# Kernel tuning notes

Measured on AMD Instinct MI355X. Metric: run time of the kernel, lower is better.

## Reference

```python
import jax, jax.numpy as jnp
import numpy as np

H = 100      # hidden/embedding size (hard-coded in the module)
HD = H // 2  # per-direction encoder hidden
V = 50000


def lstm_scan(xs, h0, c0, Wx, Wh, b):
    """xs: [T,B,E] -> (all hidden states [T,B,H], final h, final c)."""
    def step(carry, x):
        h, c = carry
        g = x @ Wx + h @ Wh + b          # [B, 4H]
        i, f, gg, o = jnp.split(g, 4, axis=-1)
        c = jax.nn.sigmoid(f) * c + jax.nn.sigmoid(i) * jnp.tanh(gg)
        h = jax.nn.sigmoid(o) * jnp.tanh(c)
        return (h, c), h
    (h, c), hs = jax.lax.scan(step, (h0, c0), xs)
    return hs, h, c


def setup_inputs() -> dict:
    key = jax.random.key(0)
    ks = jax.random.split(key, 16)
    B, S, T = 128, 512, 128
    s = 0.02
    inp = {
        "src": jax.random.randint(ks[0], (B, S), 0, V),
        "tgt": jax.random.randint(ks[1], (B, T), 0, V),
        "mask_src": jnp.ones((B, S), dtype=bool),
        "emb": jax.random.normal(ks[2], (V, H), jnp.float32) * s,
        "demb": jax.random.normal(ks[3], (V, H), jnp.float32) * s,
        "enc_Wx_f": jax.random.normal(ks[4], (H, 4 * HD), jnp.float32) * s,
        "enc_Wh_f": jax.random.normal(ks[5], (HD, 4 * HD), jnp.float32) * s,
        "enc_b_f": jnp.zeros((4 * HD,), jnp.float32),
        "enc_Wx_b": jax.random.normal(ks[6], (H, 4 * HD), jnp.float32) * s,
        "enc_Wh_b": jax.random.normal(ks[7], (HD, 4 * HD), jnp.float32) * s,
        "enc_b_b": jnp.zeros((4 * HD,), jnp.float32),
        "dec_Wx": jax.random.normal(ks[8], (H, 4 * H), jnp.float32) * s,
        "dec_Wh": jax.random.normal(ks[9], (H, 4 * H), jnp.float32) * s,
        "dec_b": jnp.zeros((4 * H,), jnp.float32),
        "Wa": jax.random.normal(ks[10], (H, H), jnp.float32) * s,
        "Wc": jax.random.normal(ks[11], (2 * H, H), jnp.float32) * s,
    }
    return inp


def reference(src, tgt, mask_src, emb, demb,
              enc_Wx_f, enc_Wh_f, enc_b_f,
              enc_Wx_b, enc_Wh_b, enc_b_b,
              dec_Wx, dec_Wh, dec_b, Wa, Wc):
    B, S = src.shape
    # ---- bidirectional LSTM encoder ----
    x = emb[src].transpose(1, 0, 2)                      # [S,B,H]
    z = jnp.zeros((B, HD), x.dtype)
    hf, hfT, cfT = lstm_scan(x, z, z, enc_Wx_f, enc_Wh_f, enc_b_f)
    hb_r, hbT, cbT = lstm_scan(x[::-1], z, z, enc_Wx_b, enc_Wh_b, enc_b_b)
    hb = hb_r[::-1]
    mem = jnp.concatenate([hf, hb], -1).transpose(1, 0, 2)  # [B,S,H] memory bank
    h0 = jnp.concatenate([hfT, hbT], -1)                 # [B,H] init decoder state
    c0 = jnp.concatenate([cfT, cbT], -1)
    # ---- LSTM decoder (teacher forcing on tgt[:, :-1]) ----
    y = demb[tgt[:, :-1]].transpose(1, 0, 2)             # [T-1,B,H]
    dh, _, _ = lstm_scan(y, h0, c0, dec_Wx, dec_Wh, dec_b)
    dh = dh.transpose(1, 0, 2)                           # [B,T-1,H]
    # ---- global (general/Luong) attention over memory bank ----
    scores = jnp.einsum('bth,hk,bsk->bts', dh, Wa, mem)  # [B,T-1,S]
    scores = jnp.where(mask_src[:, None, :], scores, -1e9)
    attn = jax.nn.softmax(scores, axis=-1)
    ctx = jnp.einsum('bts,bsh->bth', attn, mem)          # [B,T-1,H]
    decode_output = jnp.tanh(jnp.concatenate([dh, ctx], -1) @ Wc)  # [B,T-1,H]
    return decode_output, attn
```

## Files before the change

kernel.cpp:

```cpp
#include <hip/hip_runtime.h>
#include <hip/hip_bf16.h>

#define B_   128
#define S_   512
#define TM1  127
#define H_   100
#define HD_  50

__device__ __forceinline__ float sigm(float x) {
    return __fdividef(1.0f, 1.0f + __expf(-x));
}
__device__ __forceinline__ float ftanh(float x) {
    float e = __expf(2.0f * x);
    return __fdividef(e - 1.0f, e + 1.0f);
}
__device__ __forceinline__ void wave_barrier() {
    __builtin_amdgcn_sched_barrier(0);
    asm volatile("s_waitcnt lgkmcnt(0)");
    __builtin_amdgcn_sched_barrier(0);
    __builtin_amdgcn_s_barrier();
    __builtin_amdgcn_sched_barrier(0);
}

__global__ __launch_bounds__(256) void k_xg_enc(
    const int* __restrict__ src, const float* __restrict__ emb,
    const float* __restrict__ Wf, const float* __restrict__ bf,
    const float* __restrict__ Wb, const float* __restrict__ bb,
    float* __restrict__ xgfT, float* __restrict__ xgbT)
{
    __shared__ __align__(16) float a[32][100];
    __shared__ int ridx[32];
    const int tid = threadIdx.x;
    const int b   = blockIdx.x & 127;
    const int t0  = (blockIdx.x >> 7) * 32;
    if (tid < 32) ridx[tid] = src[b * S_ + t0 + tid];
    __syncthreads();
    for (int i = tid; i < 32 * 100; i += 256) {
        int rr = i / 100, k = i - rr * 100;
        a[rr][k] = emb[(size_t)ridx[rr] * 100 + k];
    }
    __syncthreads();
    #pragma unroll
    for (int pass = 0; pass < 2; ++pass) {
        int j = tid + pass * 256;
        if (j < 400) {
            const float* W; const float* bias; float* out; int jj;
            if (j < 200) { W = Wf; bias = bf; out = xgfT; jj = j; }
            else         { W = Wb; bias = bb; out = xgbT; jj = j - 200; }
            float acc[32];
            float bv = bias[jj];
            #pragma unroll
            for (int rr = 0; rr < 32; ++rr) acc[rr] = bv;
            for (int k4 = 0; k4 < 25; ++k4) {
                float w0 = W[(4 * k4 + 0) * 200 + jj];
                float w1 = W[(4 * k4 + 1) * 200 + jj];
                float w2 = W[(4 * k4 + 2) * 200 + jj];
                float w3 = W[(4 * k4 + 3) * 200 + jj];
                #pragma unroll
                for (int rr = 0; rr < 32; ++rr) {
                    float4 av = reinterpret_cast<const float4*>(a[rr])[k4];
                    acc[rr] = fmaf(av.x, w0, acc[rr]);
                    acc[rr] = fmaf(av.y, w1, acc[rr]);
                    acc[rr] = fmaf(av.z, w2, acc[rr]);
                    acc[rr] = fmaf(av.w, w3, acc[rr]);
                }
            }
            const int gate = jj / 50, uu = jj - (jj / 50) * 50;
            const int pj = uu * 4 + gate;
            float* dst = out + ((size_t)b * 200 + pj) * 512 + t0;
            #pragma unroll
            for (int q = 0; q < 8; ++q)
                *reinterpret_cast<float4*>(dst + 4 * q) =
                    make_float4(acc[4*q+0], acc[4*q+1], acc[4*q+2], acc[4*q+3]);
        }
    }
}

__global__ __launch_bounds__(256) void k_xg_dec(
    const int* __restrict__ tgt, const float* __restrict__ demb,
    const float* __restrict__ W, const float* __restrict__ bias,
    float* __restrict__ xgdT)
{
    __shared__ __align__(16) float a[32][100];
    __shared__ int ridx[32];
    const int tid = threadIdx.x;
    const int b   = blockIdx.x & 127;
    const int t0  = (blockIdx.x >> 7) * 32;
    if (tid < 32) ridx[tid] = tgt[b * 128 + t0 + tid];
    __syncthreads();
    for (int i = tid; i < 32 * 100; i += 256) {
        int rr = i / 100, k = i - rr * 100;
        a[rr][k] = demb[(size_t)ridx[rr] * 100 + k];
    }
    __syncthreads();
    #pragma unroll
    for (int pass = 0; pass < 2; ++pass) {
        int j = tid + pass * 256;
        if (j < 400) {
            float acc[32];
            float bv = bias[j];
            #pragma unroll
            for (int rr = 0; rr < 32; ++rr) acc[rr] = bv;
            for (int k4 = 0; k4 < 25; ++k4) {
                float w0 = W[(4 * k4 + 0) * 400 + j];
                float w1 = W[(4 * k4 + 1) * 400 + j];
                float w2 = W[(4 * k4 + 2) * 400 + j];
                float w3 = W[(4 * k4 + 3) * 400 + j];
                #pragma unroll
                for (int rr = 0; rr < 32; ++rr) {
                    float4 av = reinterpret_cast<const float4*>(a[rr])[k4];
                    acc[rr] = fmaf(av.x, w0, acc[rr]);
                    acc[rr] = fmaf(av.y, w1, acc[rr]);
                    acc[rr] = fmaf(av.z, w2, acc[rr]);
                    acc[rr] = fmaf(av.w, w3, acc[rr]);
                }
            }
            const int gate = j / 100, uu = j - (j / 100) * 100;
            const int pj = uu * 4 + gate;
            float* dst = xgdT + ((size_t)b * 400 + pj) * 128 + t0;
            #pragma unroll
            for (int q = 0; q < 8; ++q)
                *reinterpret_cast<float4*>(dst + 4 * q) =
                    make_float4(acc[4*q+0], acc[4*q+1], acc[4*q+2], acc[4*q+3]);
        }
    }
}

__global__ __launch_bounds__(256, 1) void k_enc(
    const float* __restrict__ xgfT, const float* __restrict__ xgbT,
    const float* __restrict__ Whf, const float* __restrict__ Whb,
    float* __restrict__ memT, float* __restrict__ h0, float* __restrict__ c0)
{
    const int blk = blockIdx.x;
    const int dir = blk >> 7;
    const int b   = blk & 127;
    const float* __restrict__ xgT = dir ? xgbT : xgfT;
    const float* __restrict__ Wh  = dir ? Whb  : Whf;
    const int tid = threadIdx.x;
    const int u    = tid >> 2;
    const int gbit = tid & 3;
    const bool active = tid < 200;
    const bool glane  = active && (gbit == 0);

    __shared__ __align__(16) float hbuf[2][56];
    __shared__ float hT[2][50][17];

    const int col = active ? (gbit * 50 + u) : 0;
    const float* wbase = Wh + col;
    float4 W0,W1,W2,W3,W4,W5,W6,W7,W8,W9,W10,W11,W12;
#define LDW(i) \
    asm volatile("global_load_dword %0, %1, off" : "=v"(W##i.x) : "v"(wbase + (4*(i)+0)*200)); \
    asm volatile("global_load_dword %0, %1, off" : "=v"(W##i.y) : "v"(wbase + (4*(i)+1)*200)); \
    asm volatile("global_load_dword %0, %1, off" : "=v"(W##i.z) : "v"(wbase + (4*(i)+2)*200)); \
    asm volatile("global_load_dword %0, %1, off" : "=v"(W##i.w) : "v"(wbase + (4*(i)+3)*200));
    LDW(0) LDW(1) LDW(2) LDW(3) LDW(4) LDW(5) LDW(6)
    LDW(7) LDW(8) LDW(9) LDW(10) LDW(11)
#undef LDW
    asm volatile("global_load_dword %0, %1, off" : "=v"(W12.x) : "v"(wbase + 48*200));
    asm volatile("global_load_dword %0, %1, off" : "=v"(W12.y) : "v"(wbase + 49*200));
    asm volatile("s_waitcnt vmcnt(0)");
    __builtin_amdgcn_sched_barrier(0);
    W12.z = 0.f; W12.w = 0.f;

    if (tid < 56) { hbuf[0][tid] = 0.f; hbuf[1][tid] = 0.f; }
    float c = 0.f;
    wave_barrier();

    const float* xrow = xgT + ((size_t)b * 200 + (active ? tid : 0)) * 512;

#define LOADQ(g_) ((active && (g_) < 128) \
    ? *reinterpret_cast<const float4*>(xrow + (dir ? (508 - 4 * (g_)) : (4 * (g_)))) \
    : make_float4(0.f, 0.f, 0.f, 0.f))

#define EDOT(i, h4) { float4 hv = (h4)[i]; \
    a0 = fmaf(hv.x, W##i.x, a0); a1 = fmaf(hv.y, W##i.y, a1); \
    a2 = fmaf(hv.z, W##i.z, a2); a3 = fmaf(hv.w, W##i.w, a3); }

#define ESTEP(s_, rb_, gx_) { \
    float gv; \
    { \
        const float4* h4 = reinterpret_cast<const float4*>(hbuf[rb_]); \
        float a0 = 0.f, a1 = 0.f, a2 = 0.f, a3 = 0.f; \
        EDOT(0, h4) EDOT(1, h4) EDOT(2, h4) EDOT(3, h4) EDOT(4, h4) \
        EDOT(5, h4) EDOT(6, h4) EDOT(7, h4) EDOT(8, h4) EDOT(9, h4) \
        EDOT(10, h4) EDOT(11, h4) EDOT(12, h4) \
        gv = (gx_) + (a0 + a1) + (a2 + a3); \
    } \
    const float x1 = __shfl_xor(gv, 1); \
    const float x2 = __shfl_xor(gv, 2); \
    const float x3 = __shfl_xor(gv, 3); \
    const int t_ = dir ? (S_ - 1 - (s_)) : (s_); \
    if (glane) { \
        c = sigm(x1) * c + sigm(gv) * ftanh(x2); \
        float h = sigm(x3) * ftanh(c); \
        hbuf[(rb_) ^ 1][u] = h; \
        hT[((s_) >> 4) & 1][u][t_ & 15] = h; \
    } \
    wave_barrier(); \
    if (((s_) & 15) == 15) { \
        const int tbase = dir ? t_ : ((s_) - 15); \
        const int par = ((s_) >> 4) & 1; \
        for (int i = tid; i < 50 * 16; i += 256) { \
            int uu = i >> 4, tt = i & 15; \
            memT[((size_t)b * 100 + dir * 50 + uu) * 512 + tbase + tt] = \
                hT[par][uu][tt]; \
        } \
    } \
}

    float4 cq = LOADQ(0);
    for (int g = 0; g < 128; ++g) {
        const int s = g * 4;
        float4 nq = LOADQ(g + 1);
        if (dir) {
            ESTEP(s + 0, 0, cq.w)
            ESTEP(s + 1, 1, cq.z)
            ESTEP(s + 2, 0, cq.y)
            ESTEP(s + 3, 1, cq.x)
        } else {
            ESTEP(s + 0, 0, cq.x)
            ESTEP(s + 1, 1, cq.y)
            ESTEP(s + 2, 0, cq.z)
            ESTEP(s + 3, 1, cq.w)
        }
        cq = nq;
    }
#undef ESTEP
#undef EDOT
#undef LOADQ
    if (glane) {
        h0[b * 100 + dir * 50 + u] = hbuf[0][u];
        c0[b * 100 + dir * 50 + u] = c;
    }
}

__global__ __launch_bounds__(832, 1) void k_dec(
    const float* __restrict__ xgdT, const float* __restrict__ Whd,
    const float* __restrict__ h0v, const float* __restrict__ c0v,
    float* __restrict__ dh)
{
    const int b   = blockIdx.x;
    const int tid = threadIdx.x;
    const int u   = tid >> 3;
    const int gt  = (tid >> 1) & 3;
    const int p   = tid & 1;
    const bool active = tid < 800;
    const bool glane  = active && ((tid & 7) == 0);

    __shared__ __align__(16) float hbuf[2][100];

    const int colD = active ? (gt * 100 + u) : 0;
    const int pofs = active ? (p * 50) : 0;
    float2 V0,V1,V2,V3,V4,V5,V6,V7,V8,V9,V10,V11,V12,
           V13,V14,V15,V16,V17,V18,V19,V20,V21,V22,V23,V24;
#define LDV(i) V##i = make_float2(Whd[(size_t)(pofs + 2*i    ) * 400 + colD], \
                                  Whd[(size_t)(pofs + 2*i + 1) * 400 + colD]);
    LDV(0) LDV(1) LDV(2) LDV(3) LDV(4) LDV(5) LDV(6) LDV(7) LDV(8) LDV(9)
    LDV(10) LDV(11) LDV(12) LDV(13) LDV(14) LDV(15) LDV(16) LDV(17) LDV(18)
    LDV(19) LDV(20) LDV(21) LDV(22) LDV(23) LDV(24)
#undef LDV

    if (tid < 100) hbuf[0][tid] = h0v[b * 100 + tid];
    float c = 0.f;
    if (glane) c = c0v[b * 100 + u];
    wave_barrier();

    const float* xrow = xgdT + ((size_t)b * 400 + (tid >> 1)) * 128;

#define LOADQD(g_) ((active && p == 0 && (g_) < 32) \
    ? *reinterpret_cast<const float4*>(xrow + 4 * (g_)) \
    : make_float4(0.f, 0.f, 0.f, 0.f))

#define DDOT(i, h2) { float2 hv = (h2)[i]; \
    a0 = fmaf(hv.x, V##i.x, a0); a1 = fmaf(hv.y, V##i.y, a1); }

#define DSTEP(s_, rb_, gx_) { \
    float pv; \
    { \
        const float2* h2 = reinterpret_cast<const float2*>(hbuf[rb_] + p * 50); \
        float a0 = 0.f, a1 = 0.f; \
        DDOT(0, h2) DDOT(1, h2) DDOT(2, h2) DDOT(3, h2) DDOT(4, h2) \
        DDOT(5, h2) DDOT(6, h2) DDOT(7, h2) DDOT(8, h2) DDOT(9, h2) \
        DDOT(10, h2) DDOT(11, h2) DDOT(12, h2) DDOT(13, h2) DDOT(14, h2) \
        DDOT(15, h2) DDOT(16, h2) DDOT(17, h2) DDOT(18, h2) DDOT(19, h2) \
        DDOT(20, h2) DDOT(21, h2) DDOT(22, h2) DDOT(23, h2) DDOT(24, h2) \
        pv = a0 + a1; \
    } \
    pv += __shfl_xor(pv, 1); \
    const float gv = (gx_) + pv; \
    const float x2 = __shfl_xor(gv, 2); \
    const float x4 = __shfl_xor(gv, 4); \
    const float x6 = __shfl_xor(gv, 6); \
    if (glane) { \
        c = sigm(x2) * c + sigm(gv) * ftanh(x4); \
        float h = sigm(x6) * ftanh(c); \
        hbuf[(rb_) ^ 1][u] = h; \
        dh[((size_t)(s_) * 128 + b) * 100 + u] = h; \
    } \
    wave_barrier(); \
}

    float4 q0 = LOADQD(0);
    float4 q1 = LOADQD(1);
    int s = 0;
    for (int g = 0; g < 31; ++g) {
        float4 qc = q0; q0 = q1; q1 = LOADQD(g + 2);
        DSTEP(s + 0, 0, qc.x)
        DSTEP(s + 1, 1, qc.y)
        DSTEP(s + 2, 0, qc.z)
        DSTEP(s + 3, 1, qc.w)
        s += 4;
    }
    DSTEP(s + 0, 0, q0.x)
    DSTEP(s + 1, 1, q0.y)
    DSTEP(s + 2, 0, q0.z)
#undef DSTEP
#undef DDOT
#undef LOADQD
}

__global__ __launch_bounds__(128) void k_dhwa(
    const float* __restrict__ dh, const float* __restrict__ Wa,
    float* __restrict__ out)
{
    __shared__ __align__(16) float a[32][100];
    const int tid = threadIdx.x;
    const size_t r0 = (size_t)blockIdx.x * 32;
    for (int i = tid; i < 32 * 100; i += 128) {
        int rr = i / 100, k = i - rr * 100;
        a[rr][k] = dh[(r0 + rr) * 100 + k];
    }
    __syncthreads();
    if (tid < 100) {
        float acc[32];
        #pragma unroll
        for (int rr = 0; rr < 32; ++rr) acc[rr] = 0.f;
        for (int k4 = 0; k4 < 25; ++k4) {
            float w0 = Wa[(4 * k4 + 0) * 100 + tid];
            float w1 = Wa[(4 * k4 + 1) * 100 + tid];
            float w2 = Wa[(4 * k4 + 2) * 100 + tid];
            float w3 = Wa[(4 * k4 + 3) * 100 + tid];
            #pragma unroll
            for (int rr = 0; rr < 32; ++rr) {
                float4 av = reinterpret_cast<const float4*>(a[rr])[k4];
                acc[rr] = fmaf(av.x, w0, acc[rr]);
                acc[rr] = fmaf(av.y, w1, acc[rr]);
                acc[rr] = fmaf(av.z, w2, acc[rr]);
                acc[rr] = fmaf(av.w, w3, acc[rr]);
            }
        }
        #pragma unroll
        for (int rr = 0; rr < 32; ++rr) out[(r0 + rr) * 100 + tid] = acc[rr];
    }
}

__global__ __launch_bounds__(256) void k_attn(
    const float* __restrict__ dhWa, const float* __restrict__ memT,
    float* __restrict__ attn_out, float* __restrict__ ctx)
{
    const int tid = threadIdx.x;
    const int b   = blockIdx.x & 127;
    const int t0  = (blockIdx.x >> 7) * 8;
    const int nt  = (TM1 - t0 < 8) ? (TM1 - t0) : 8;
    __shared__ __align__(16) float q[8][100];
    __shared__ __align__(16) float p[8][512];
    __shared__ float redm[4][8];
    __shared__ float reds[4][8];
    for (int i = tid; i < 8 * 100; i += 256) {
        int rr = i / 100, k = i - rr * 100;
        q[rr][k] = (rr < nt) ? dhWa[((size_t)(t0 + rr) * 128 + b) * 100 + k] : 0.0f;
    }
    __syncthreads();
    float acc0[8], acc1[8];
    #pragma unroll
    for (int rr = 0; rr < 8; ++rr) { acc0[rr] = 0.f; acc1[rr] = 0.f; }
    const float* mb = memT + (size_t)b * 100 * 512;
    for (int k4 = 0; k4 < 25; ++k4) {
        float qs[8][4];
        #pragma unroll
        for (int rr = 0; rr < 8; ++rr) {
            float4 v = reinterpret_cast<const float4*>(q[rr])[k4];
            qs[rr][0] = v.x; qs[rr][1] = v.y; qs[rr][2] = v.z; qs[rr][3] = v.w;
        }
        #pragma unroll
        for (int uu = 0; uu < 4; ++uu) {
            const float* col = mb + (size_t)(4 * k4 + uu) * 512;
            float m0 = col[tid], m1 = col[tid + 256];
            #pragma unroll
            for (int rr = 0; rr < 8; ++rr) {
                acc0[rr] = fmaf(qs[rr][uu], m0, acc0[rr]);
                acc1[rr] = fmaf(qs[rr][uu], m1, acc1[rr]);
            }
        }
    }
    const int wid = tid >> 6;
    #pragma unroll
    for (int rr = 0; rr < 8; ++rr) {
        float m = fmaxf(acc0[rr], acc1[rr]);
        #pragma unroll
        for (int k = 1; k < 64; k <<= 1) m = fmaxf(m, __shfl_xor(m, k));
        if ((tid & 63) == 0) redm[wid][rr] = m;
    }
    __syncthreads();
    #pragma unroll
    for (int rr = 0; rr < 8; ++rr) {
        float m = fmaxf(fmaxf(redm[0][rr], redm[1][rr]),
                        fmaxf(redm[2][rr], redm[3][rr]));
        acc0[rr] = __expf(acc0[rr] - m);
        acc1[rr] = __expf(acc1[rr] - m);
        float s = acc0[rr] + acc1[rr];
        #pragma unroll
        for (int k = 1; k < 64; k <<= 1) s += __shfl_xor(s, k);
        if ((tid & 63) == 0) reds[wid][rr] = s;
    }
    __syncthreads();
    #pragma unroll
    for (int rr = 0; rr < 8; ++rr) {
        float s = (reds[0][rr] + reds[1][rr]) + (reds[2][rr] + reds[3][rr]);
        float inv = __fdividef(1.0f, s);
        float e0 = acc0[rr] * inv, e1 = acc1[rr] * inv;
        p[rr][tid] = e0; p[rr][tid + 256] = e1;
        if (rr < nt) {
            float* ao = attn_out + ((size_t)b * TM1 + t0 + rr) * 512;
            ao[tid] = e0; ao[tid + 256] = e1;
        }
    }
    __syncthreads();
    if (tid < 200) {
        const int h  = (tid < 100) ? tid : tid - 100;
        const int r0 = (tid < 100) ? 0 : 4;
        const float4* mrow = reinterpret_cast<const float4*>(mb + (size_t)h * 512);
        const float4* p0 = reinterpret_cast<const float4*>(p[r0 + 0]);
        const float4* p1 = reinterpret_cast<const float4*>(p[r0 + 1]);
        const float4* p2 = reinterpret_cast<const float4*>(p[r0 + 2]);
        const float4* p3 = reinterpret_cast<const float4*>(p[r0 + 3]);
        float a0 = 0.f, a1 = 0.f, a2 = 0.f, a3 = 0.f;
        for (int s4 = 0; s4 < 128; ++s4) {
            float4 mv = mrow[s4];
            float4 v0 = p0[s4], v1 = p1[s4], v2 = p2[s4], v3 = p3[s4];
            a0 = fmaf(v0.x, mv.x, a0); a0 = fmaf(v0.y, mv.y, a0);
            a0 = fmaf(v0.z, mv.z, a0); a0 = fmaf(v0.w, mv.w, a0);
            a1 = fmaf(v1.x, mv.x, a1); a1 = fmaf(v1.y, mv.y, a1);
            a1 = fmaf(v1.z, mv.z, a1); a1 = fmaf(v1.w, mv.w, a1);
            a2 = fmaf(v2.x, mv.x, a2); a2 = fmaf(v2.y, mv.y, a2);
            a2 = fmaf(v2.z, mv.z, a2); a2 = fmaf(v2.w, mv.w, a2);
            a3 = fmaf(v3.x, mv.x, a3); a3 = fmaf(v3.y, mv.y, a3);
            a3 = fmaf(v3.z, mv.z, a3); a3 = fmaf(v3.w, mv.w, a3);
        }
        float av[4] = {a0, a1, a2, a3};
        #pragma unroll
        for (int k = 0; k < 4; ++k) {
            int rr = r0 + k;
            if (rr < nt)
                ctx[((size_t)b * TM1 + t0 + rr) * 100 + h] = av[k];
        }
    }
}

__global__ __launch_bounds__(128) void k_final(
    const float* __restrict__ dh, const float* __restrict__ ctx,
    const float* __restrict__ Wc, float* __restrict__ outp)
{
    __shared__ __align__(16) float a[32][200];
    const int tid = threadIdx.x;
    const int r0 = blockIdx.x * 32;
    for (int i = tid; i < 32 * 200; i += 128) {
        int rr = i / 200, k = i - rr * 200;
        int r = r0 + rr; int bb = r / 127; int t = r - bb * 127;
        a[rr][k] = (k < 100) ? dh[((size_t)t * 128 + bb) * 100 + k]
                             : ctx[(size_t)r * 100 + (k - 100)];
    }
    __syncthreads();
    if (tid < 100) {
        float acc[32];
        #pragma unroll
        for (int rr = 0; rr < 32; ++rr) acc[rr] = 0.f;
        for (int k4 = 0; k4 < 50; ++k4) {
            float w0 = Wc[(4 * k4 + 0) * 100 + tid];
            float w1 = Wc[(4 * k4 + 1) * 100 + tid];
            float w2 = Wc[(4 * k4 + 2) * 100 + tid];
            float w3 = Wc[(4 * k4 + 3) * 100 + tid];
            #pragma unroll
            for (int rr = 0; rr < 32; ++rr) {
                float4 av = reinterpret_cast<const float4*>(a[rr])[k4];
                acc[rr] = fmaf(av.x, w0, acc[rr]);
                acc[rr] = fmaf(av.y, w1, acc[rr]);
                acc[rr] = fmaf(av.z, w2, acc[rr]);
                acc[rr] = fmaf(av.w, w3, acc[rr]);
            }
        }
        #pragma unroll
        for (int rr = 0; rr < 32; ++rr)
            outp[(size_t)(r0 + rr) * 100 + tid] = tanhf(acc[rr]);
    }
}

extern "C" void kernel_launch(void* const* d_in, const int* in_sizes, int n_in,
                              void* d_out, int out_size, void* d_ws, size_t ws_size,
                              hipStream_t stream) {
    const int*   src  = (const int*)d_in[0];
    const int*   tgt  = (const int*)d_in[1];
    const float* emb  = (const float*)d_in[3];
    const float* demb = (const float*)d_in[4];
    const float* Wxf  = (const float*)d_in[5];
    const float* Whf  = (const float*)d_in[6];
    const float* bf   = (const float*)d_in[7];
    const float* Wxb  = (const float*)d_in[8];
    const float* Whb  = (const float*)d_in[9];
    const float* bb   = (const float*)d_in[10];
    const float* Wxd  = (const float*)d_in[11];
    const float* Whd  = (const float*)d_in[12];
    const float* bd   = (const float*)d_in[13];
    const float* Wa   = (const float*)d_in[14];
    const float* Wc   = (const float*)d_in[15];

    float* ws    = (float*)d_ws;
    float* xgfT  = ws;
    float* xgbT  = xgfT + 13107200;
    float* xgdT  = xgbT + 13107200;
    float* memT  = xgdT + 6553600;
    float* h0    = memT + 6553600;
    float* c0    = h0 + 12800;
    float* dh    = ws;
    float* dhwa  = dh + 1625600;
    float* ctx   = dhwa + 1625600;

    float* out_dec  = (float*)d_out;
    float* out_attn = out_dec + 1625600;

    k_xg_enc<<<2048, 256, 0, stream>>>(src, emb, Wxf, bf, Wxb, bb, xgfT, xgbT);
    k_xg_dec<<<512, 256, 0, stream>>>(tgt, demb, Wxd, bd, xgdT);
    k_enc<<<256, 256, 0, stream>>>(xgfT, xgbT, Whf, Whb, memT, h0, c0);
    k_dec<<<128, 832, 0, stream>>>(xgdT, Whd, h0, c0, dh);
    k_dhwa<<<508, 128, 0, stream>>>(dh, Wa, dhwa);
    k_attn<<<2048, 256, 0, stream>>>(dhwa, memT, out_attn, ctx);
    k_final<<<508, 128, 0, stream>>>(dh, ctx, Wc, out_dec);
}
```

Baseline: 854.9 us.

## Fuse dh@Wa projection into attention kernel and merge projection passes per thread

The separate k_dhwa kernel is removed. Each attention block now computes its own 8-row dh·Wa query tile in shared memory before scoring, which drops one launch and the round trip of the intermediate through global memory. The input-gate projection kernels also change from two passes over 256 threads to one pass over 200 threads, each computing two output columns, so every shared-memory activation load feeds twice as many FMAs. The cost is higher register pressure (64 accumulators per thread), 56 idle threads per block, and a small amount of extra serial work at the start of each attention block.

Result: faster. 809.0 us (-5.4%).

```diff
diff --git a/kernel.cpp b/kernel.cpp
--- a/kernel.cpp
+++ b/kernel.cpp
@@ -40,38 +40,44 @@
         a[rr][k] = emb[(size_t)ridx[rr] * 100 + k];
     }
     __syncthreads();
-    #pragma unroll
-    for (int pass = 0; pass < 2; ++pass) {
-        int j = tid + pass * 256;
-        if (j < 400) {
-            const float* W; const float* bias; float* out; int jj;
-            if (j < 200) { W = Wf; bias = bf; out = xgfT; jj = j; }
-            else         { W = Wb; bias = bb; out = xgbT; jj = j - 200; }
-            float acc[32];
-            float bv = bias[jj];
-            #pragma unroll
-            for (int rr = 0; rr < 32; ++rr) acc[rr] = bv;
-            for (int k4 = 0; k4 < 25; ++k4) {
-                float w0 = W[(4 * k4 + 0) * 200 + jj];
-                float w1 = W[(4 * k4 + 1) * 200 + jj];
-                float w2 = W[(4 * k4 + 2) * 200 + jj];
-                float w3 = W[(4 * k4 + 3) * 200 + jj];
-                #pragma unroll
-                for (int rr = 0; rr < 32; ++rr) {
-                    float4 av = reinterpret_cast<const float4*>(a[rr])[k4];
-                    acc[rr] = fmaf(av.x, w0, acc[rr]);
-                    acc[rr] = fmaf(av.y, w1, acc[rr]);
-                    acc[rr] = fmaf(av.z, w2, acc[rr]);
-                    acc[rr] = fmaf(av.w, w3, acc[rr]);
-                }
+    if (tid < 200) {
+        const int jj = tid;
+        float accF[32], accB[32];
+        const float bvF = bf[jj], bvB = bb[jj];
+        #pragma unroll
+        for (int rr = 0; rr < 32; ++rr) { accF[rr] = bvF; accB[rr] = bvB; }
+        for (int k4 = 0; k4 < 25; ++k4) {
+            float f0 = Wf[(4 * k4 + 0) * 200 + jj];
+            float f1 = Wf[(4 * k4 + 1) * 200 + jj];
+            float f2 = Wf[(4 * k4 + 2) * 200 + jj];
+            float f3 = Wf[(4 * k4 + 3) * 200 + jj];
+            float g0 = Wb[(4 * k4 + 0) * 200 + jj];
+            float g1 = Wb[(4 * k4 + 1) * 200 + jj];
+            float g2 = Wb[(4 * k4 + 2) * 200 + jj];
+            float g3 = Wb[(4 * k4 + 3) * 200 + jj];
+            #pragma unroll
+            for (int rr = 0; rr < 32; ++rr) {
+                float4 av = reinterpret_cast<const float4*>(a[rr])[k4];
+                accF[rr] = fmaf(av.x, f0, accF[rr]);
+                accF[rr] = fmaf(av.y, f1, accF[rr]);
+                accF[rr] = fmaf(av.z, f2, accF[rr]);
+                accF[rr] = fmaf(av.w, f3, accF[rr]);
+                accB[rr] = fmaf(av.x, g0, accB[rr]);
+                accB[rr] = fmaf(av.y, g1, accB[rr]);
+                accB[rr] = fmaf(av.z, g2, accB[rr]);
+                accB[rr] = fmaf(av.w, g3, accB[rr]);
             }
-            const int gate = jj / 50, uu = jj - (jj / 50) * 50;
-            const int pj = uu * 4 + gate;
-            float* dst = out + ((size_t)b * 200 + pj) * 512 + t0;
-            #pragma unroll
-            for (int q = 0; q < 8; ++q)
-                *reinterpret_cast<float4*>(dst + 4 * q) =
-                    make_float4(acc[4*q+0], acc[4*q+1], acc[4*q+2], acc[4*q+3]);
+        }
+        const int gate = jj / 50, uu = jj - (jj / 50) * 50;
+        const int pj = uu * 4 + gate;
+        float* dstF = xgfT + ((size_t)b * 200 + pj) * 512 + t0;
+        float* dstB = xgbT + ((size_t)b * 200 + pj) * 512 + t0;
+        #pragma unroll
+        for (int q = 0; q < 8; ++q) {
+            *reinterpret_cast<float4*>(dstF + 4 * q) =
+                make_float4(accF[4*q+0], accF[4*q+1], accF[4*q+2], accF[4*q+3]);
+            *reinterpret_cast<float4*>(dstB + 4 * q) =
+                make_float4(accB[4*q+0], accB[4*q+1], accB[4*q+2], accB[4*q+3]);
         }
     }
 }
@@ -93,35 +99,49 @@
         a[rr][k] = demb[(size_t)ridx[rr] * 100 + k];
     }
     __syncthreads();
-    #pragma unroll
-    for (int pass = 0; pass < 2; ++pass) {
-        int j = tid + pass * 256;
-        if (j < 400) {
-            float acc[32];
-            float bv = bias[j];
-            #pragma unroll
-            for (int rr = 0; rr < 32; ++rr) acc[rr] = bv;
-            for (int k4 = 0; k4 < 25; ++k4) {
-                float w0 = W[(4 * k4 + 0) * 400 + j];
-                float w1 = W[(4 * k4 + 1) * 400 + j];
-                float w2 = W[(4 * k4 + 2) * 400 + j];
-                float w3 = W[(4 * k4 + 3) * 400 + j];
-                #pragma unroll
-                for (int rr = 0; rr < 32; ++rr) {
-                    float4 av = reinterpret_cast<const float4*>(a[rr])[k4];
-                    acc[rr] = fmaf(av.x, w0, acc[rr]);
-                    acc[rr] = fmaf(av.y, w1, acc[rr]);
-                    acc[rr] = fmaf(av.z, w2, acc[rr]);
-                    acc[rr] = fmaf(av.w, w3, acc[rr]);
-                }
+    if (tid < 200) {
+        const int j0 = tid, j1 = tid + 200;
+        float acc0[32], acc1[32];
+        const float bv0 = bias[j0], bv1 = bias[j1];
+        #pragma unroll
+        for (int rr = 0; rr < 32; ++rr) { acc0[rr] = bv0; acc1[rr] = bv1; }
+        for (int k4 = 0; k4 < 25; ++k4) {
+            float f0 = W[(4 * k4 + 0) * 400 + j0];
+            float f1 = W[(4 * k4 + 1) * 400 + j0];
+            float f2 = W[(4 * k4 + 2) * 400 + j0];
+            float f3 = W[(4 * k4 + 3) * 400 + j0];
+            float g0 = W[(4 * k4 + 0) * 400 + j1];
+            float g1 = W[(4 * k4 + 1) * 400 + j1];
+            float g2 = W[(4 * k4 + 2) * 400 + j1];
+            float g3 = W[(4 * k4 + 3) * 400 + j1];
+            #pragma unroll
+            for (int rr = 0; rr < 32; ++rr) {
+                float4 av = reinterpret_cast<const float4*>(a[rr])[k4];
+                acc0[rr] = fmaf(av.x, f0, acc0[rr]);
+                acc0[rr] = fmaf(av.y, f1, acc0[rr]);
+                acc0[rr] = fmaf(av.z, f2, acc0[rr]);
+                acc0[rr] = fmaf(av.w, f3, acc0[rr]);
+                acc1[rr] = fmaf(av.x, g0, acc1[rr]);
+                acc1[rr] = fmaf(av.y, g1, acc1[rr]);
+                acc1[rr] = fmaf(av.z, g2, acc1[rr]);
+                acc1[rr] = fmaf(av.w, g3, acc1[rr]);
             }
-            const int gate = j / 100, uu = j - (j / 100) * 100;
-            const int pj = uu * 4 + gate;
-            float* dst = xgdT + ((size_t)b * 400 + pj) * 128 + t0;
+        }
+        {
+            const int gate = j0 / 100, uu = j0 - (j0 / 100) * 100;
+            float* dst = xgdT + ((size_t)b * 400 + uu * 4 + gate) * 128 + t0;
             #pragma unroll
             for (int q = 0; q < 8; ++q)
                 *reinterpret_cast<float4*>(dst + 4 * q) =
-                    make_float4(acc[4*q+0], acc[4*q+1], acc[4*q+2], acc[4*q+3]);
+                    make_float4(acc0[4*q+0], acc0[4*q+1], acc0[4*q+2], acc0[4*q+3]);
+        }
+        {
+            const int gate = j1 / 100, uu = j1 - (j1 / 100) * 100;
+            float* dst = xgdT + ((size_t)b * 400 + uu * 4 + gate) * 128 + t0;
+            #pragma unroll
+            for (int q = 0; q < 8; ++q)
+                *reinterpret_cast<float4*>(dst + 4 * q) =
+                    make_float4(acc1[4*q+0], acc1[4*q+1], acc1[4*q+2], acc1[4*q+3]);
         }
     }
 }
@@ -319,56 +339,45 @@
 #undef LOADQD
 }
 
-__global__ __launch_bounds__(128) void k_dhwa(
+__global__ __launch_bounds__(256) void k_attn(
     const float* __restrict__ dh, const float* __restrict__ Wa,
-    float* __restrict__ out)
-{
-    __shared__ __align__(16) float a[32][100];
-    const int tid = threadIdx.x;
-    const size_t r0 = (size_t)blockIdx.x * 32;
-    for (int i = tid; i < 32 * 100; i += 128) {
-        int rr = i / 100, k = i - rr * 100;
-        a[rr][k] = dh[(r0 + rr) * 100 + k];
-    }
-    __syncthreads();
-    if (tid < 100) {
-        float acc[32];
-        #pragma unroll
-        for (int rr = 0; rr < 32; ++rr) acc[rr] = 0.f;
-        for (int k4 = 0; k4 < 25; ++k4) {
-            float w0 = Wa[(4 * k4 + 0) * 100 + tid];
-            float w1 = Wa[(4 * k4 + 1) * 100 + tid];
-            float w2 = Wa[(4 * k4 + 2) * 100 + tid];
-            float w3 = Wa[(4 * k4 + 3) * 100 + tid];
-            #pragma unroll
-            for (int rr = 0; rr < 32; ++rr) {
-                float4 av = reinterpret_cast<const float4*>(a[rr])[k4];
-                acc[rr] = fmaf(av.x, w0, acc[rr]);
-                acc[rr] = fmaf(av.y, w1, acc[rr]);
-                acc[rr] = fmaf(av.z, w2, acc[rr]);
-                acc[rr] = fmaf(av.w, w3, acc[rr]);
-            }
-        }
-        #pragma unroll
-        for (int rr = 0; rr < 32; ++rr) out[(r0 + rr) * 100 + tid] = acc[rr];
-    }
-}
-
-__global__ __launch_bounds__(256) void k_attn(
-    const float* __restrict__ dhWa, const float* __restrict__ memT,
+    const float* __restrict__ memT,
     float* __restrict__ attn_out, float* __restrict__ ctx)
 {
     const int tid = threadIdx.x;
     const int b   = blockIdx.x & 127;
     const int t0  = (blockIdx.x >> 7) * 8;
     const int nt  = (TM1 - t0 < 8) ? (TM1 - t0) : 8;
+    __shared__ __align__(16) float dtile[8][100];
     __shared__ __align__(16) float q[8][100];
     __shared__ __align__(16) float p[8][512];
     __shared__ float redm[4][8];
     __shared__ float reds[4][8];
     for (int i = tid; i < 8 * 100; i += 256) {
         int rr = i / 100, k = i - rr * 100;
-        q[rr][k] = (rr < nt) ? dhWa[((size_t)(t0 + rr) * 128 + b) * 100 + k] : 0.0f;
+        dtile[rr][k] = (rr < nt) ? dh[((size_t)(t0 + rr) * 128 + b) * 100 + k] : 0.0f;
+    }
+    __syncthreads();
+    if (tid < 100) {
+        float qa[8];
+        #pragma unroll
+        for (int rr = 0; rr < 8; ++rr) qa[rr] = 0.f;
+        for (int k4 = 0; k4 < 25; ++k4) {
+            float w0 = Wa[(4 * k4 + 0) * 100 + tid];
+            float w1 = Wa[(4 * k4 + 1) * 100 + tid];
+            float w2 = Wa[(4 * k4 + 2) * 100 + tid];
+            float w3 = Wa[(4 * k4 + 3) * 100 + tid];
+            #pragma unroll
+            for (int rr = 0; rr < 8; ++rr) {
+                float4 av = reinterpret_cast<const float4*>(dtile[rr])[k4];
+                qa[rr] = fmaf(av.x, w0, qa[rr]);
+                qa[rr] = fmaf(av.y, w1, qa[rr]);
+                qa[rr] = fmaf(av.z, w2, qa[rr]);
+                qa[rr] = fmaf(av.w, w3, qa[rr]);
+            }
+        }
+        #pragma unroll
+        for (int rr = 0; rr < 8; ++rr) q[rr][tid] = qa[rr];
     }
     __syncthreads();
     float acc0[8], acc1[8];
@@ -522,8 +531,7 @@
     float* h0    = memT + 6553600;
     float* c0    = h0 + 12800;
     float* dh    = ws;
-    float* dhwa  = dh + 1625600;
-    float* ctx   = dhwa + 1625600;
+    float* ctx   = dh + 2 * 1625600;
 
     float* out_dec  = (float*)d_out;
     float* out_attn = out_dec + 1625600;
@@ -532,7 +540,6 @@
     k_xg_dec<<<512, 256, 0, stream>>>(tgt, demb, Wxd, bd, xgdT);
     k_enc<<<256, 256, 0, stream>>>(xgfT, xgbT, Whf, Whb, memT, h0, c0);
     k_dec<<<128, 832, 0, stream>>>(xgdT, Whd, h0, c0, dh);
-    k_dhwa<<<508, 128, 0, stream>>>(dh, Wa, dhwa);
-    k_attn<<<2048, 256, 0, stream>>>(dhwa, memT, out_attn, ctx);
+    k_attn<<<2048, 256, 0, stream>>>(dh, Wa, memT, out_attn, ctx);
     k_final<<<508, 128, 0, stream>>>(dh, ctx, Wc, out_dec);
 }
```
